# Kernel optimization log

Hardware: AMD Instinct MI355X
Metric: run time of the kernel (lower is better)

## Reference

```python
import jax, jax.numpy as jnp
import numpy as np

H, W, DIM, B, K = 28, 28, 384, 64, 1
EPS = 1e-5


def setup_inputs() -> dict:
    key = jax.random.key(0)
    k1, k2, k3 = jax.random.split(key, 3)
    L = 1 + K * H * W
    x = jax.random.normal(k1, (B, L, DIM), dtype=jnp.float32)
    w_reduction = jax.random.normal(k2, (2 * DIM, 4 * DIM), dtype=jnp.float32) * 0.02
    w_convert = jax.random.normal(k3, (2 * DIM, DIM), dtype=jnp.float32) * 0.02
    ln_gamma = jnp.ones((4 * DIM,), dtype=jnp.float32)
    ln_beta = jnp.zeros((4 * DIM,), dtype=jnp.float32)
    return {"x": x, "w_reduction": w_reduction, "w_convert": w_convert,
            "ln_gamma": ln_gamma, "ln_beta": ln_beta}


def reference(x, w_reduction, w_convert, ln_gamma, ln_beta):
    Bb, L, C = x.shape
    k = (L - 1) // (H * W)
    cls_token = x[:, 0:1, :]                      # [B,1,C]
    feat = x[:, 1:, :].reshape(Bb, k, H, W, C)
    x0 = feat[:, :, 0::2, 0::2, :]                # [B,k,H/2,W/2,C]
    x1 = feat[:, :, 1::2, 0::2, :]
    x2 = feat[:, :, 0::2, 1::2, :]
    x3 = feat[:, :, 1::2, 1::2, :]
    m = jnp.concatenate([x0, x1, x2, x3], axis=-1)  # [B,k,H/2,W/2,4C]
    m = m.reshape(Bb, k, -1, 4 * C)
    # LayerNorm over last dim
    mu = jnp.mean(m, axis=-1, keepdims=True)
    var = jnp.mean(jnp.square(m - mu), axis=-1, keepdims=True)
    m = (m - mu) * jax.lax.rsqrt(var + EPS) * ln_gamma + ln_beta
    red = jnp.einsum('bknf,of->bkno', m, w_reduction).reshape(Bb, -1, 2 * C)
    cls_out = jnp.einsum('bic,oc->bio', cls_token, w_convert)  # [B,1,2C]
    return jnp.concatenate([cls_out, red], axis=1)
```

## Files before the change

### kernel.cpp

```cpp
#include <hip/hip_runtime.h>
#include <hip/hip_bf16.h>

#define DIMC 384
#define LL 785
#define FDIM 1536
#define ODIM 768
#define NPATCH 196
#define MROWS 12544
#define BATCH 64

typedef __attribute__((ext_vector_type(8))) short bf16x8;
typedef __attribute__((ext_vector_type(4))) float floatx4;
typedef __attribute__((ext_vector_type(4))) unsigned short ushort4v;

#define WS_WBF_OFF  38535168
#define WS_PST_OFF  40894464
#define WS_B2_OFF   41295872

#define PB_CLS   0
#define PB_CAST  192
#define PB_BIAS  1760
#define PB_WBF   1952
#define PREP_BLOCKS 3104

__device__ __forceinline__ unsigned short f2bf(float f) {
  union { float f; unsigned int u; } v; v.f = f;
  unsigned int u = v.u + 0x7fffu + ((v.u >> 16) & 1u);
  return (unsigned short)(u >> 16);
}

__device__ __forceinline__ void gload_lds16(const void* g, void* l) {
  __builtin_amdgcn_global_load_lds(
      (const __attribute__((address_space(1))) unsigned int*)g,
      (__attribute__((address_space(3))) unsigned int*)l, 16, 0, 0);
}

__global__ __launch_bounds__(256) void prep_kernel(
    const float* __restrict__ x, const float* __restrict__ wred,
    const float* __restrict__ wconv, const float* __restrict__ gamma,
    const float* __restrict__ beta, unsigned short* __restrict__ xbf,
    unsigned short* __restrict__ wbf, float2* __restrict__ pst,
    float2* __restrict__ bias2, float* __restrict__ out) {
  const int blk = blockIdx.x;
  const int t = threadIdx.x;
  const int wv = t >> 6;
  const int lane = t & 63;

  if (blk >= PB_CAST && blk < PB_BIAS) {
    const int w = (blk - PB_CAST) * 4 + wv;
    const int vid0 = w * 8 + (lane >> 4) * 2;
    const int sub = lane & 15;
    float4 v[2][6];
    float s[2], s2[2];
#pragma unroll
    for (int r = 0; r < 2; ++r) {
      int vid = vid0 + r;
      int b = vid / 784;
      int ll = vid - b * 784;
      const float* src = x + ((size_t)b * LL + 1 + ll) * DIMC;
      s[r] = 0.f; s2[r] = 0.f;
#pragma unroll
      for (int c = 0; c < 6; ++c) {
        float4 vv = *reinterpret_cast<const float4*>(src + sub * 4 + c * 64);
        v[r][c] = vv;
        s[r]  += vv.x + vv.y + vv.z + vv.w;
        s2[r] += vv.x * vv.x + vv.y * vv.y + vv.z * vv.z + vv.w * vv.w;
      }
    }
#pragma unroll
    for (int r = 0; r < 2; ++r) {
      unsigned short* dst = xbf + (size_t)(vid0 + r) * DIMC;
#pragma unroll
      for (int c = 0; c < 6; ++c) {
        float4 vv = v[r][c];
        union { ushort4v u4; __hip_bfloat162 h[2]; } u;
        u.h[0] = __float22bfloat162_rn(make_float2(vv.x, vv.y));
        u.h[1] = __float22bfloat162_rn(make_float2(vv.z, vv.w));
        *reinterpret_cast<ushort4v*>(dst + sub * 4 + c * 64) = u.u4;
      }
    }
#pragma unroll
    for (int o = 1; o < 16; o <<= 1) {
#pragma unroll
      for (int r = 0; r < 2; ++r) {
        s[r]  += __shfl_xor(s[r], o);
        s2[r] += __shfl_xor(s2[r], o);
      }
    }
    if (sub == 0) {
      float4 pp = make_float4(s[0], s2[0], s[1], s2[1]);
      *reinterpret_cast<float4*>(&pst[vid0]) = pp;
    }
  } else if (blk < PB_CAST) {
    __shared__ float xs[DIMC];
    int idx = blk;
    int b = idx / 3;
    int ch = idx - b * 3;
    for (int c = t; c < DIMC; c += 256) xs[c] = x[(size_t)b * LL * DIMC + c];
    __syncthreads();
    int o = ch * 256 + t;
    const float* wr = wconv + (size_t)o * DIMC;
    float a0 = 0.f, a1 = 0.f;
#pragma unroll 4
    for (int c = 0; c < DIMC; c += 8) {
      float4 w0 = *reinterpret_cast<const float4*>(wr + c);
      float4 w1 = *reinterpret_cast<const float4*>(wr + c + 4);
      float4 p0 = *reinterpret_cast<const float4*>(&xs[c]);
      float4 p1 = *reinterpret_cast<const float4*>(&xs[c + 4]);
      a0 += w0.x * p0.x + w0.y * p0.y + w0.z * p0.z + w0.w * p0.w;
      a1 += w1.x * p1.x + w1.y * p1.y + w1.z * p1.z + w1.w * p1.w;
    }
    out[(size_t)b * 197 * ODIM + o] = a0 + a1;
  } else if (blk < PB_WBF) {
    int o = (blk - PB_BIAS) * 4 + wv;
    const float* wr = wred + (size_t)o * FDIM;
    float sb = 0.f, sg = 0.f;
#pragma unroll
    for (int c = 0; c < 6; ++c) {
      int f = lane * 4 + c * 256;
      float4 w = *reinterpret_cast<const float4*>(wr + f);
      float4 be = *reinterpret_cast<const float4*>(beta + f);
      float4 ga = *reinterpret_cast<const float4*>(gamma + f);
      sb += w.x * be.x + w.y * be.y + w.z * be.z + w.w * be.w;
      sg += w.x * ga.x + w.y * ga.y + w.z * ga.z + w.w * ga.w;
    }
#pragma unroll
    for (int o2 = 32; o2 > 0; o2 >>= 1) {
      sb += __shfl_down(sb, o2);
      sg += __shfl_down(sg, o2);
    }
    if (lane == 0) bias2[o] = make_float2(sg, sb);
  } else {
    int idx4 = (blk - PB_WBF) * 256 + t;
    int e0 = idx4 * 4;
    int f = e0 % FDIM;
    float4 w = *reinterpret_cast<const float4*>(wred + e0);
    float4 g = *reinterpret_cast<const float4*>(gamma + f);
    ushort4v u;
    u.x = f2bf(w.x * g.x); u.y = f2bf(w.y * g.y);
    u.z = f2bf(w.z * g.z); u.w = f2bf(w.w * g.w);
    *reinterpret_cast<ushort4v*>(wbf + e0) = u;
  }
}

__global__ __launch_bounds__(256) void gemm_kernel(
    const unsigned short* __restrict__ xbf,
    const unsigned short* __restrict__ wbf,
    const float2* __restrict__ pst, const float2* __restrict__ bias2,
    float* __restrict__ out) {
  __shared__ unsigned short As[128 * 64];
  __shared__ unsigned short Bs[64 * 64];
  __shared__ float2 st[128];

  const int t = threadIdx.x;

  int bid = blockIdx.x;
  int wg = (bid & 7) * 147 + (bid >> 3);
  int my = wg / 12;
  int nx = wg - my * 12;
  const int mBase = my * 128;
  const int nBase = nx * 64;

  if (t < 128) {
    int m = mBase + t;
    int b = m / NPATCH;
    int n = m - b * NPATCH;
    int i = n / 14;
    int j = n - i * 14;
    int base = b * 784 + i * 56 + j * 2;
    float2 p0 = pst[base];
    float2 p1 = pst[base + 28];
    float2 p2 = pst[base + 1];
    float2 p3 = pst[base + 29];
    float s = p0.x + p1.x + p2.x + p3.x;
    float s2 = p0.y + p1.y + p2.y + p3.y;
    float mu = s * (1.f / FDIM);
    float var = s2 * (1.f / FDIM) - mu * mu;
    float rs = rsqrtf(var + 1e-5f);
    st[t] = make_float2(rs, -mu * rs);
  }

  const unsigned short* agp[4];
  const unsigned short* bgp[2];
  unsigned int aldso[4], bldso[2];
#pragma unroll
  for (int p = 0; p < 4; ++p) {
    int s = p * 256 + t;
    int r = s >> 3;
    int cs = (s & 7) ^ (r & 7);
    int m = mBase + r;
    int b = m / NPATCH;
    int n = m - b * NPATCH;
    int i = n / 14;
    int j = n - i * 14;
    agp[p] = xbf + ((size_t)b * 784 + i * 56 + j * 2) * DIMC + cs * 8;
    aldso[p] = (unsigned)s * 8;
  }
#pragma unroll
  for (int p = 0; p < 2; ++p) {
    int s = p * 256 + t;
    int r = s >> 3;
    int cs = (s & 7) ^ (r & 7);
    bgp[p] = wbf + (size_t)(nBase + r) * FDIM + cs * 8;
    bldso[p] = (unsigned)s * 8;
  }

  const int wv = t >> 6;
  const int lane = t & 63;
  const int ln15 = lane & 15;
  const int quad = lane >> 4;
  const int wm = wv >> 1;
  const int wn = wv & 1;

  unsigned int aoff[4][2], boff[2][2];
#pragma unroll
  for (int mt = 0; mt < 4; ++mt)
#pragma unroll
    for (int h = 0; h < 2; ++h) {
      int rA = wm * 64 + mt * 16 + ln15;
      aoff[mt][h] = (unsigned)(rA * 64 + (((h * 4 + quad) ^ (rA & 7)) * 8));
    }
#pragma unroll
  for (int nt = 0; nt < 2; ++nt)
#pragma unroll
    for (int h = 0; h < 2; ++h) {
      int rB = wn * 32 + nt * 16 + ln15;
      boff[nt][h] = (unsigned)(rB * 64 + (((h * 4 + quad) ^ (rB & 7)) * 8));
    }

  floatx4 acc[4][2];
#pragma unroll
  for (int mt = 0; mt < 4; ++mt)
#pragma unroll
    for (int nt = 0; nt < 2; ++nt)
      acc[mt][nt] = floatx4{0.f, 0.f, 0.f, 0.f};

  for (int kt = 0; kt < FDIM / 64; ++kt) {
    int q = kt / 6;
    int kk = kt - q * 6;
    int ao = ((q & 1) * 28 + ((q >> 1) & 1)) * DIMC + kk * 64;
    if (kt) __syncthreads();
#pragma unroll
    for (int p = 0; p < 4; ++p)
      gload_lds16(agp[p] + ao, &As[aldso[p]]);
#pragma unroll
    for (int p = 0; p < 2; ++p) {
      gload_lds16(bgp[p], &Bs[bldso[p]]);
      bgp[p] += 64;
    }
    __syncthreads();

#pragma unroll
    for (int h = 0; h < 2; ++h) {
      bf16x8 af[4], bfr[2];
#pragma unroll
      for (int mt = 0; mt < 4; ++mt)
        af[mt] = *reinterpret_cast<const bf16x8*>(&As[aoff[mt][h]]);
#pragma unroll
      for (int nt = 0; nt < 2; ++nt)
        bfr[nt] = *reinterpret_cast<const bf16x8*>(&Bs[boff[nt][h]]);
#pragma unroll
      for (int mt = 0; mt < 4; ++mt)
#pragma unroll
        for (int nt = 0; nt < 2; ++nt)
          acc[mt][nt] = __builtin_amdgcn_mfma_f32_16x16x32_bf16(
              af[mt], bfr[nt], acc[mt][nt], 0, 0, 0);
    }
  }

  float2 gb[2];
#pragma unroll
  for (int nt = 0; nt < 2; ++nt)
    gb[nt] = bias2[nBase + wn * 32 + nt * 16 + ln15];
#pragma unroll
  for (int mt = 0; mt < 4; ++mt) {
#pragma unroll
    for (int r = 0; r < 4; ++r) {
      int rloc = wm * 64 + mt * 16 + quad * 4 + r;
      float2 sn = st[rloc];
      int m = mBase + rloc;
      int b = m / NPATCH;
      int n = m - b * NPATCH;
      float* orow = out + ((size_t)b * 197 + 1 + n) * ODIM + nBase + wn * 32;
#pragma unroll
      for (int nt = 0; nt < 2; ++nt) {
        float val = fmaf(acc[mt][nt][r], sn.x,
                         fmaf(sn.y, gb[nt].x, gb[nt].y));
        __builtin_nontemporal_store(val, &orow[nt * 16 + ln15]);
      }
    }
  }
}

extern "C" void kernel_launch(void* const* d_in, const int* in_sizes, int n_in,
                              void* d_out, int out_size, void* d_ws, size_t ws_size,
                              hipStream_t stream) {
  const float* x     = (const float*)d_in[0];
  const float* wred  = (const float*)d_in[1];
  const float* wconv = (const float*)d_in[2];
  const float* gamma = (const float*)d_in[3];
  const float* beta  = (const float*)d_in[4];
  float* out = (float*)d_out;

  unsigned short* xbf = (unsigned short*)d_ws;
  unsigned short* wbf = (unsigned short*)((char*)d_ws + WS_WBF_OFF);
  float2* pst         = (float2*)((char*)d_ws + WS_PST_OFF);
  float2* bias2       = (float2*)((char*)d_ws + WS_B2_OFF);

  prep_kernel<<<dim3(PREP_BLOCKS), 256, 0, stream>>>(x, wred, wconv, gamma,
                                                     beta, xbf, wbf, pst,
                                                     bias2, out);
  gemm_kernel<<<dim3(1176), 256, 0, stream>>>(xbf, wbf, pst, bias2, out);
}
```

Measured before the change: 178.1 us.

## Use 128x128 GEMM tiles with double-buffered K=32 LDS pipeline

The GEMM tile grows from 128x64 to 128x128, so each wave computes a 64x64 sub-tile with 16 accumulators, and the grid shrinks to 588 workgroups. The K loop now steps by 32 with two LDS buffers: the next slice's global-to-LDS loads are issued before the MFMAs on the current slice, leaving one barrier per step. The XCD-aware block remap is generalized to the new workgroup count. The aim is better operand reuse and overlap of loads with compute, at the cost of more accumulator registers, twice as many K iterations and barriers, and fewer workgroups to fill the GPU.

```diff
diff --git a/kernel.cpp b/kernel.cpp
--- a/kernel.cpp
+++ b/kernel.cpp
@@ -148,18 +148,22 @@
     const unsigned short* __restrict__ wbf,
     const float2* __restrict__ pst, const float2* __restrict__ bias2,
     float* __restrict__ out) {
-  __shared__ unsigned short As[128 * 64];
-  __shared__ unsigned short Bs[64 * 64];
+  __shared__ unsigned short As[2][64 * 64];
+  __shared__ unsigned short Bs[2][64 * 64];
   __shared__ float2 st[128];
 
   const int t = threadIdx.x;
 
+  const int NWG = (ODIM / 128) * (MROWS / 128);
+  const int qq = NWG >> 3, rr = NWG & 7;
   int bid = blockIdx.x;
-  int wg = (bid & 7) * 147 + (bid >> 3);
-  int my = wg / 12;
-  int nx = wg - my * 12;
+  int xcd = bid & 7, pos = bid >> 3;
+  int wg = (xcd < rr) ? xcd * (qq + 1) + pos
+                      : rr * (qq + 1) + (xcd - rr) * qq + pos;
+  int my = wg / 6;
+  int nx = wg - my * 6;
   const int mBase = my * 128;
-  const int nBase = nx * 64;
+  const int nBase = nx * 128;
 
   if (t < 128) {
     int m = mBase + t;
@@ -180,29 +184,24 @@
     st[t] = make_float2(rs, -mu * rs);
   }
 
-  const unsigned short* agp[4];
+  const unsigned short* agp[2];
   const unsigned short* bgp[2];
-  unsigned int aldso[4], bldso[2];
-#pragma unroll
-  for (int p = 0; p < 4; ++p) {
+  unsigned int ldso[2];
+#pragma unroll
+  for (int p = 0; p < 2; ++p) {
     int s = p * 256 + t;
-    int r = s >> 3;
-    int cs = (s & 7) ^ (r & 7);
+    int rho = s >> 3;
+    int g = (s & 7) ^ (rho & 7);
+    int r = rho + ((g >> 2) << 6);
+    int kc = g & 3;
     int m = mBase + r;
     int b = m / NPATCH;
     int n = m - b * NPATCH;
     int i = n / 14;
     int j = n - i * 14;
-    agp[p] = xbf + ((size_t)b * 784 + i * 56 + j * 2) * DIMC + cs * 8;
-    aldso[p] = (unsigned)s * 8;
-  }
-#pragma unroll
-  for (int p = 0; p < 2; ++p) {
-    int s = p * 256 + t;
-    int r = s >> 3;
-    int cs = (s & 7) ^ (r & 7);
-    bgp[p] = wbf + (size_t)(nBase + r) * FDIM + cs * 8;
-    bldso[p] = (unsigned)s * 8;
+    agp[p] = xbf + ((size_t)b * 784 + i * 56 + j * 2) * DIMC + kc * 8;
+    bgp[p] = wbf + (size_t)(nBase + r) * FDIM + kc * 8;
+    ldso[p] = (unsigned)s * 8;
   }
 
   const int wv = t >> 6;
@@ -212,66 +211,61 @@
   const int wm = wv >> 1;
   const int wn = wv & 1;
 
-  unsigned int aoff[4][2], boff[2][2];
+  unsigned int aoff[4], boff[4];
+#pragma unroll
+  for (int mt = 0; mt < 4; ++mt) {
+    int rho = mt * 16 + ln15;
+    aoff[mt] = (unsigned)(rho * 64 + (((wm * 4 + quad) ^ (rho & 7)) * 8));
+    boff[mt] = (unsigned)(rho * 64 + (((wn * 4 + quad) ^ (rho & 7)) * 8));
+  }
+
+  floatx4 acc[4][4];
 #pragma unroll
   for (int mt = 0; mt < 4; ++mt)
 #pragma unroll
-    for (int h = 0; h < 2; ++h) {
-      int rA = wm * 64 + mt * 16 + ln15;
-      aoff[mt][h] = (unsigned)(rA * 64 + (((h * 4 + quad) ^ (rA & 7)) * 8));
-    }
-#pragma unroll
-  for (int nt = 0; nt < 2; ++nt)
-#pragma unroll
-    for (int h = 0; h < 2; ++h) {
-      int rB = wn * 32 + nt * 16 + ln15;
-      boff[nt][h] = (unsigned)(rB * 64 + (((h * 4 + quad) ^ (rB & 7)) * 8));
-    }
-
-  floatx4 acc[4][2];
-#pragma unroll
-  for (int mt = 0; mt < 4; ++mt)
-#pragma unroll
-    for (int nt = 0; nt < 2; ++nt)
+    for (int nt = 0; nt < 4; ++nt)
       acc[mt][nt] = floatx4{0.f, 0.f, 0.f, 0.f};
 
-  for (int kt = 0; kt < FDIM / 64; ++kt) {
-    int q = kt / 6;
-    int kk = kt - q * 6;
-    int ao = ((q & 1) * 28 + ((q >> 1) & 1)) * DIMC + kk * 64;
-    if (kt) __syncthreads();
-#pragma unroll
-    for (int p = 0; p < 4; ++p)
-      gload_lds16(agp[p] + ao, &As[aldso[p]]);
-#pragma unroll
-    for (int p = 0; p < 2; ++p) {
-      gload_lds16(bgp[p], &Bs[bldso[p]]);
-      bgp[p] += 64;
-    }
+#pragma unroll
+  for (int p = 0; p < 2; ++p) {
+    gload_lds16(agp[p], &As[0][ldso[p]]);
+    gload_lds16(bgp[p], &Bs[0][ldso[p]]);
+  }
+  __syncthreads();
+
+  int nq = 0, nkk = 0;
+  for (int kt = 0; kt < FDIM / 32; ++kt) {
+    const int cur = kt & 1;
+    if (kt + 1 < FDIM / 32) {
+      if (++nkk == 12) { nkk = 0; ++nq; }
+      int ao = ((nq & 1) * 28 + ((nq >> 1) & 1)) * DIMC + nkk * 32;
+#pragma unroll
+      for (int p = 0; p < 2; ++p) {
+        gload_lds16(agp[p] + ao, &As[cur ^ 1][ldso[p]]);
+        bgp[p] += 32;
+        gload_lds16(bgp[p], &Bs[cur ^ 1][ldso[p]]);
+      }
+    }
+    bf16x8 af[4], bfr[4];
+#pragma unroll
+    for (int mt = 0; mt < 4; ++mt)
+      af[mt] = *reinterpret_cast<const bf16x8*>(&As[cur][aoff[mt]]);
+#pragma unroll
+    for (int nt = 0; nt < 4; ++nt)
+      bfr[nt] = *reinterpret_cast<const bf16x8*>(&Bs[cur][boff[nt]]);
+#pragma unroll
+    for (int mt = 0; mt < 4; ++mt)
+#pragma unroll
+      for (int nt = 0; nt < 4; ++nt)
+        acc[mt][nt] = __builtin_amdgcn_mfma_f32_16x16x32_bf16(
+            af[mt], bfr[nt], acc[mt][nt], 0, 0, 0);
     __syncthreads();
-
-#pragma unroll
-    for (int h = 0; h < 2; ++h) {
-      bf16x8 af[4], bfr[2];
-#pragma unroll
-      for (int mt = 0; mt < 4; ++mt)
-        af[mt] = *reinterpret_cast<const bf16x8*>(&As[aoff[mt][h]]);
-#pragma unroll
-      for (int nt = 0; nt < 2; ++nt)
-        bfr[nt] = *reinterpret_cast<const bf16x8*>(&Bs[boff[nt][h]]);
-#pragma unroll
-      for (int mt = 0; mt < 4; ++mt)
-#pragma unroll
-        for (int nt = 0; nt < 2; ++nt)
-          acc[mt][nt] = __builtin_amdgcn_mfma_f32_16x16x32_bf16(
-              af[mt], bfr[nt], acc[mt][nt], 0, 0, 0);
-    }
-  }
-
-  float2 gb[2];
-#pragma unroll
-  for (int nt = 0; nt < 2; ++nt)
-    gb[nt] = bias2[nBase + wn * 32 + nt * 16 + ln15];
+  }
+
+  float2 gb[4];
+#pragma unroll
+  for (int nt = 0; nt < 4; ++nt)
+    gb[nt] = bias2[nBase + wn * 64 + nt * 16 + ln15];
 #pragma unroll
   for (int mt = 0; mt < 4; ++mt) {
 #pragma unroll
@@ -281,9 +275,9 @@
       int m = mBase + rloc;
       int b = m / NPATCH;
       int n = m - b * NPATCH;
-      float* orow = out + ((size_t)b * 197 + 1 + n) * ODIM + nBase + wn * 32;
-#pragma unroll
-      for (int nt = 0; nt < 2; ++nt) {
+      float* orow = out + ((size_t)b * 197 + 1 + n) * ODIM + nBase + wn * 64;
+#pragma unroll
+      for (int nt = 0; nt < 4; ++nt) {
         float val = fmaf(acc[mt][nt][r], sn.x,
                          fmaf(sn.y, gb[nt].x, gb[nt].y));
         __builtin_nontemporal_store(val, &orow[nt * 16 + ln15]);
@@ -310,5 +304,6 @@
   prep_kernel<<<dim3(PREP_BLOCKS), 256, 0, stream>>>(x, wred, wconv, gamma,
                                                      beta, xbf, wbf, pst,
                                                      bias2, out);
-  gemm_kernel<<<dim3(1176), 256, 0, stream>>>(xbf, wbf, pst, bias2, out);
-}
+  gemm_kernel<<<dim3((ODIM / 128) * (MROWS / 128)), 256, 0, stream>>>(
+      xbf, wbf, pst, bias2, out);
+}
```

After: 196.6 us. +10.4%, slower.
